# Kernel optimization log

Hardware: AMD Instinct MI355X
Metric: run time of the kernel (lower is better)

The kernel has to match this reference:

```python
import jax, jax.numpy as jnp
import numpy as np


def setup_inputs() -> dict:
    key = jax.random.key(0)
    x = jax.random.normal(key, (4096, 4096), dtype=jnp.float32)
    return {"x": x}


def reference(x):
    """IDXST: y_k = Im{ sum_{n=0}^{N-1} x_n * exp(j*pi*n*(2k+1)/(2N)) }.

    O(N log N) via a 2N-point FFT:
      sum_n x_n e^{j pi n (2k+1)/(2N)} = sum_n (x_n e^{j pi n/(2N)}) e^{j 2 pi n k/(2N)}
    which is the first N entries of an unnormalized 2N-point inverse DFT of the
    twiddled, zero-padded sequence.
    """
    N = x.shape[-1]
    n = jnp.arange(N)
    twiddle = jnp.exp(1j * jnp.pi * n.astype(jnp.float32) / (2.0 * N)).astype(jnp.complex64)
    c = x.astype(jnp.complex64) * twiddle                      # [..., N]
    pad = [(0, 0)] * (x.ndim - 1) + [(0, N)]
    c = jnp.pad(c, pad)                                        # [..., 2N]
    y = jnp.fft.ifft(c, axis=-1) * (2.0 * N)                   # unnormalized IDFT
    return jnp.imag(y[..., :N]).astype(x.dtype)
```

## Files before the change

kernel.cpp:

```cpp
#include <hip/hip_runtime.h>
#include <stdint.h>


#define NN 4096

typedef __attribute__((ext_vector_type(8))) short short8;
typedef __attribute__((ext_vector_type(4))) float f32x4;

__device__ __forceinline__ unsigned short f2bf(float f) {
  unsigned int u = __float_as_uint(f);
  u += 0x7fffu + ((u >> 16) & 1u);
  return (unsigned short)(u >> 16);
}

__device__ __forceinline__ void async_load16(const void* g, void* lds) {
  __builtin_amdgcn_global_load_lds(
      (const __attribute__((address_space(1))) unsigned int*)g,
      (__attribute__((address_space(3))) unsigned int*)lds, 16, 0, 0);
}

#define NXS (NN * NN / 8)
#define NBO (2048 * 2048 / 4)
#define NBP (1024 * 1024 / 4)

__global__ void prep_kernel(const float* __restrict__ x,
                            unsigned short* __restrict__ xo,
                            unsigned short* __restrict__ xee,
                            unsigned short* __restrict__ xeo,
                            unsigned short* __restrict__ Bo,
                            unsigned short* __restrict__ Bp,
                            unsigned short* __restrict__ Bq) {
  int gi = blockIdx.x * blockDim.x + threadIdx.x;
  if (gi < NXS) {
    int g = gi & 511;
    int r = gi >> 9;
    const float4* src = (const float4*)(x + (size_t)r * NN + g * 8);
    float4 v0 = src[0], v1 = src[1];
    ushort4 ov;
    ov.x = f2bf(v0.y); ov.y = f2bf(v0.w); ov.z = f2bf(v1.y); ov.w = f2bf(v1.w);
    *(ushort4*)&xo[(size_t)r * 2048 + g * 4] = ov;
    unsigned int ee = ((unsigned)f2bf(v1.x) << 16) | f2bf(v0.x);
    *(unsigned int*)&xee[(size_t)r * 1024 + g * 2] = ee;
    unsigned int eo = ((unsigned)f2bf(v1.z) << 16) | f2bf(v0.z);
    *(unsigned int*)&xeo[(size_t)r * 1024 + g * 2] = eo;
  } else if (gi < NXS + NBO) {
    int i = gi - NXS;
    int m0 = (i & 511) * 4;
    int c = i >> 9;
    unsigned int tw = 2u * (unsigned)c + 1u;
    const float sc = 3.14159265358979323846f / 8192.0f;
    ushort4 o; unsigned int ph;
    ph = ((unsigned)(2 * (m0 + 0) + 1) * tw) & 16383u; o.x = f2bf(__sinf((float)ph * sc));
    ph = ((unsigned)(2 * (m0 + 1) + 1) * tw) & 16383u; o.y = f2bf(__sinf((float)ph * sc));
    ph = ((unsigned)(2 * (m0 + 2) + 1) * tw) & 16383u; o.z = f2bf(__sinf((float)ph * sc));
    ph = ((unsigned)(2 * (m0 + 3) + 1) * tw) & 16383u; o.w = f2bf(__sinf((float)ph * sc));
    *(ushort4*)&Bo[(size_t)c * 2048 + m0] = o;
  } else if (gi < NXS + NBO + NBP) {
    int i = gi - NXS - NBO;
    int t0 = (i & 255) * 4;
    int c = i >> 8;
    unsigned int tw = 2u * (unsigned)c + 1u;
    const float sc = 3.14159265358979323846f / 2048.0f;
    ushort4 o; unsigned int ph;
    ph = ((unsigned)(t0 + 0) * tw) & 4095u; o.x = f2bf(__sinf((float)ph * sc));
    ph = ((unsigned)(t0 + 1) * tw) & 4095u; o.y = f2bf(__sinf((float)ph * sc));
    ph = ((unsigned)(t0 + 2) * tw) & 4095u; o.z = f2bf(__sinf((float)ph * sc));
    ph = ((unsigned)(t0 + 3) * tw) & 4095u; o.w = f2bf(__sinf((float)ph * sc));
    *(ushort4*)&Bp[(size_t)c * 1024 + t0] = o;
  } else {
    int i = gi - NXS - NBO - NBP;
    int t0 = (i & 255) * 4;
    int c = i >> 8;
    unsigned int tw = 2u * (unsigned)c + 1u;
    const float sc = 3.14159265358979323846f / 4096.0f;
    ushort4 o; unsigned int ph;
    ph = ((unsigned)(2 * (t0 + 0) + 1) * tw) & 8191u; o.x = f2bf(__sinf((float)ph * sc));
    ph = ((unsigned)(2 * (t0 + 1) + 1) * tw) & 8191u; o.y = f2bf(__sinf((float)ph * sc));
    ph = ((unsigned)(2 * (t0 + 2) + 1) * tw) & 8191u; o.z = f2bf(__sinf((float)ph * sc));
    ph = ((unsigned)(2 * (t0 + 3) + 1) * tw) & 8191u; o.w = f2bf(__sinf((float)ph * sc));
    *(ushort4*)&Bq[(size_t)c * 1024 + t0] = o;
  }
}

#define PH_BAR  __builtin_amdgcn_s_barrier()
#define W_LGKM0 asm volatile("s_waitcnt lgkmcnt(0)" ::: "memory")
#define W_VM5   asm volatile("s_waitcnt vmcnt(5)" ::: "memory")
#define W_VM0   asm volatile("s_waitcnt vmcnt(0)" ::: "memory")
#define PRIO1   __builtin_amdgcn_s_setprio(1)
#define PRIO0   __builtin_amdgcn_s_setprio(0)

#define STAGEA_G(Abase, Kc, prow0, koff, off) do {                              \
    const unsigned short* _s =                                                  \
        (Abase) + (size_t)((prow0) + st_r) * (Kc) + (koff) + st_c;              \
    async_load16(_s, &lds[(off) + tid * 8]);                                    \
    async_load16(_s + (size_t)64 * (Kc), &lds[(off) + 4096 + tid * 8]);         \
  } while (0)

#define STAGEB_P(srcp, koff, off)                                               \
    async_load16((srcp) + (koff), &lds[(off) + tid * 8])

#define LOADA_G(base, b, mh) do {                                               \
    const int _ab = (base) + (b) * 16384 + wm * 4096 + (mh) * 2048 + lr * 64;   \
    _Pragma("unroll") for (int _i = 0; _i < 2; ++_i) {                          \
      av[(mh) * 2 + _i][0] = *(const short8*)&lds[_ab + _i * 1024 + cA0];       \
      av[(mh) * 2 + _i][1] = *(const short8*)&lds[_ab + _i * 1024 + cA1];       \
    }                                                                           \
  } while (0)

#define LOADB_U(SET, nh) do {                                                   \
    const int _bb = 65536 + wn * 4096 + (nh) * 2048 + lr * 64;                  \
    _Pragma("unroll") for (int _j = 0; _j < 2; ++_j) {                          \
      SET[_j][0] = *(const short8*)&lds[_bb + _j * 1024 + cA0];                 \
      SET[_j][1] = *(const short8*)&lds[_bb + _j * 1024 + cA1];                 \
    }                                                                           \
  } while (0)

#define LOADB_PQ(SET, base) do {                                                \
    const int _bb = (base) + wn * 2048 + lr * 64;                               \
    _Pragma("unroll") for (int _j = 0; _j < 2; ++_j) {                          \
      SET[_j][0] = *(const short8*)&lds[_bb + _j * 1024 + cA0];                 \
      SET[_j][1] = *(const short8*)&lds[_bb + _j * 1024 + cA1];                 \
    }                                                                           \
  } while (0)

#define MMAQ_U(BS, mh, nh) do {                                                 \
    _Pragma("unroll") for (int _k = 0; _k < 2; ++_k)                            \
    _Pragma("unroll") for (int _i = 0; _i < 2; ++_i)                            \
    _Pragma("unroll") for (int _j = 0; _j < 2; ++_j)                            \
      uacc[(mh) * 2 + _i][(nh) * 2 + _j] =                                      \
          __builtin_amdgcn_mfma_f32_16x16x32_bf16(                              \
              av[(mh) * 2 + _i][_k], BS[_j][_k],                                \
              uacc[(mh) * 2 + _i][(nh) * 2 + _j], 0, 0, 0);                     \
  } while (0)

#define MMAQ_PQ(ACC, BS, mh) do {                                               \
    _Pragma("unroll") for (int _k = 0; _k < 2; ++_k)                            \
    _Pragma("unroll") for (int _i = 0; _i < 2; ++_i)                            \
    _Pragma("unroll") for (int _j = 0; _j < 2; ++_j)                            \
      ACC[(mh) * 2 + _i][_j] =                                                  \
          __builtin_amdgcn_mfma_f32_16x16x32_bf16(                              \
              av[(mh) * 2 + _i][_k], BS[_j][_k],                                \
              ACC[(mh) * 2 + _i][_j], 0, 0, 0);                                 \
  } while (0)

__global__ __launch_bounds__(512) void gemm3_kernel(
    const unsigned short* __restrict__ xo,
    const unsigned short* __restrict__ xee,
    const unsigned short* __restrict__ xeo,
    const unsigned short* __restrict__ Bo,
    const unsigned short* __restrict__ Bp,
    const unsigned short* __restrict__ Bq,
    float* __restrict__ out) {
  __shared__ __align__(16) unsigned short lds[73728];

  const int bx = blockIdx.x;
  const int row0 = (bx & 15) * 256;
  const int c0 = (bx >> 4) * 32;

  const int tid = threadIdx.x;
  const int lane = tid & 63;
  const int wave = tid >> 6;
  const int wm = wave >> 1;
  const int wn = wave & 1;
  const int lr = lane & 15, kq = lane >> 4;
  const int st_r = tid >> 3;
  const int st_c = ((tid & 7) ^ (st_r & 7)) * 8;
  const int cA0 = (kq ^ (lr & 7)) * 8;
  const int cA1 = ((4 + kq) ^ (lr & 7)) * 8;

  const int ru0 = (st_r < 32) ? (c0 + st_r) : (2047 - c0 - (st_r - 32));
  const int ru1 = (st_r < 32) ? (1023 - c0 - st_r) : (1024 + c0 + (st_r - 32));
  const int rpq = (st_r < 32) ? (c0 + st_r) : (1023 - c0 - (st_r - 32));
  const unsigned short* sBo0 = Bo + (size_t)ru0 * 2048 + st_c;
  const unsigned short* sBo1 = Bo + (size_t)ru1 * 2048 + st_c;
  const unsigned short* sBp  = Bp + (size_t)rpq * 1024 + st_c;
  const unsigned short* sBq  = Bq + (size_t)rpq * 1024 + st_c;

  f32x4 uacc[4][4], pacc[4][2], qacc[4][2];
#pragma unroll
  for (int i = 0; i < 4; ++i) {
#pragma unroll
    for (int j = 0; j < 4; ++j) uacc[i][j] = (f32x4){0.f, 0.f, 0.f, 0.f};
#pragma unroll
    for (int j = 0; j < 2; ++j) {
      pacc[i][j] = (f32x4){0.f, 0.f, 0.f, 0.f};
      qacc[i][j] = (f32x4){0.f, 0.f, 0.f, 0.f};
    }
  }
  short8 av[4][2], bv0[2][2], bv1[2][2];

  STAGEA_G(xo, 2048, row0,       0, 0);
  STAGEA_G(xo, 2048, row0 + 128, 0, 8192);
  STAGEB_P(sBo0, 0, 65536);
  STAGEB_P(sBo1, 0, 69632);
  W_VM0; PH_BAR;

  for (int it = 0; it < 15; ++it) {
    const int t64 = it << 7;
    LOADA_G(0, 0, 0); LOADB_U(bv0, 0);
    STAGEA_G(xo, 2048, row0, t64 + 64, 16384);
    PH_BAR; W_LGKM0; PRIO1; MMAQ_U(bv0, 0, 0); PRIO0; PH_BAR;
    LOADB_U(bv1, 1);
    STAGEA_G(xo, 2048, row0 + 128, t64 + 64, 24576);
    PH_BAR; W_LGKM0; PRIO1; MMAQ_U(bv1, 0, 1); PRIO0; PH_BAR;
    LOADA_G(0, 0, 1);
    STAGEB_P(sBo0, t64 + 64, 65536);
    STAGEB_P(sBo1, t64 + 64, 69632);
    PH_BAR; W_LGKM0; PRIO1; MMAQ_U(bv1, 1, 1); PRIO0; PH_BAR;
    PRIO1; MMAQ_U(bv0, 1, 0); PRIO0; W_VM0; PH_BAR;
    LOADA_G(0, 1, 0); LOADB_U(bv0, 0);
    STAGEA_G(xo, 2048, row0, t64 + 128, 0);
    PH_BAR; W_LGKM0; PRIO1; MMAQ_U(bv0, 0, 0); PRIO0; PH_BAR;
    LOADB_U(bv1, 1);
    STAGEA_G(xo, 2048, row0 + 128, t64 + 128, 8192);
    PH_BAR; W_LGKM0; PRIO1; MMAQ_U(bv1, 0, 1); PRIO0; PH_BAR;
    LOADA_G(0, 1, 1);
    STAGEB_P(sBo0, t64 + 128, 65536);
    STAGEB_P(sBo1, t64 + 128, 69632);
    PH_BAR; W_LGKM0; PRIO1; MMAQ_U(bv1, 1, 1); PRIO0; PH_BAR;
    PRIO1; MMAQ_U(bv0, 1, 0); PRIO0; W_VM0; PH_BAR;
  }
  {
    LOADA_G(0, 0, 0); LOADB_U(bv0, 0);
    STAGEA_G(xo, 2048, row0, 1984, 16384);
    PH_BAR; W_LGKM0; PRIO1; MMAQ_U(bv0, 0, 0); PRIO0; PH_BAR;
    LOADB_U(bv1, 1);
    STAGEA_G(xo, 2048, row0 + 128, 1984, 24576);
    PH_BAR; W_LGKM0; PRIO1; MMAQ_U(bv1, 0, 1); PRIO0; PH_BAR;
    LOADA_G(0, 0, 1);
    STAGEB_P(sBo0, 1984, 65536);
    STAGEB_P(sBo1, 1984, 69632);
    PH_BAR; W_LGKM0; PRIO1; MMAQ_U(bv1, 1, 1); PRIO0; PH_BAR;
    PRIO1; MMAQ_U(bv0, 1, 0); PRIO0; W_VM0; PH_BAR;
    LOADA_G(0, 1, 0); LOADB_U(bv0, 0);
    W_LGKM0; PRIO1; MMAQ_U(bv0, 0, 0); PRIO0;
    LOADB_U(bv1, 1);
    W_LGKM0; PRIO1; MMAQ_U(bv1, 0, 1); PRIO0;
    LOADA_G(0, 1, 1);
    W_LGKM0; PRIO1; MMAQ_U(bv1, 1, 1); MMAQ_U(bv0, 1, 0); PRIO0;
  }

  PH_BAR;
  STAGEA_G(xee, 1024, row0,       0, 0);
  STAGEA_G(xee, 1024, row0 + 128, 0, 8192);
  STAGEB_P(sBp, 0, 65536);
  STAGEA_G(xeo, 1024, row0,       0, 32768);
  STAGEA_G(xeo, 1024, row0 + 128, 0, 40960);
  STAGEB_P(sBq, 0, 69632);
  W_VM5; PH_BAR;

#define PQ_TILE(b, kn) do {                                                     \
    LOADA_G(0, b, 0); LOADB_PQ(bv0, 65536);                                     \
    STAGEA_G(xee, 1024, row0, kn, ((b) ^ 1) * 16384);                           \
    PH_BAR; W_LGKM0; PRIO1; MMAQ_PQ(pacc, bv0, 0); PRIO0; PH_BAR;               \
    LOADA_G(0, b, 1);                                                           \
    STAGEA_G(xee, 1024, row0 + 128, kn, ((b) ^ 1) * 16384 + 8192);              \
    STAGEB_P(sBp, kn, 65536);                                                   \
    PH_BAR; W_LGKM0; PRIO1; MMAQ_PQ(pacc, bv0, 1); PRIO0; W_VM5; PH_BAR;        \
    LOADA_G(32768, b, 0); LOADB_PQ(bv1, 69632);                                 \
    STAGEA_G(xeo, 1024, row0, kn, 32768 + ((b) ^ 1) * 16384);                   \
    PH_BAR; W_LGKM0; PRIO1; MMAQ_PQ(qacc, bv1, 0); PRIO0; PH_BAR;               \
    LOADA_G(32768, b, 1);                                                       \
    STAGEA_G(xeo, 1024, row0 + 128, kn, 32768 + ((b) ^ 1) * 16384 + 8192);      \
    STAGEB_P(sBq, kn, 69632);                                                   \
    PH_BAR; W_LGKM0; PRIO1; MMAQ_PQ(qacc, bv1, 1); PRIO0; W_VM5; PH_BAR;        \
  } while (0)

  for (int it = 0; it < 7; ++it) {
    const int t64 = it << 7;
    PQ_TILE(0, t64 + 64);
    PQ_TILE(1, t64 + 128);
  }
  PQ_TILE(0, 960);
  {
    LOADA_G(0, 1, 0); LOADB_PQ(bv0, 65536);
    W_LGKM0; PRIO1; MMAQ_PQ(pacc, bv0, 0); PRIO0;
    LOADA_G(0, 1, 1);
    W_LGKM0; PRIO1; MMAQ_PQ(pacc, bv0, 1); PRIO0; W_VM0; PH_BAR;
    LOADA_G(32768, 1, 0); LOADB_PQ(bv1, 69632);
    W_LGKM0; PRIO1; MMAQ_PQ(qacc, bv1, 0); PRIO0;
    LOADA_G(32768, 1, 1);
    W_LGKM0; PRIO1; MMAQ_PQ(qacc, bv1, 1); PRIO0;
  }
#undef PQ_TILE

#pragma unroll
  for (int i = 0; i < 4; ++i)
#pragma unroll
    for (int j = 0; j < 2; ++j)
#pragma unroll
      for (int rr = 0; rr < 4; ++rr) {
        const int r_out = row0 + wm * 64 + i * 16 + kq * 4 + rr;
        float* orow = out + (size_t)r_out * NN;
        const int cs = j * 16 + lr;
        const float u1 = uacc[i][j][rr];
        const float u4 = uacc[i][j + 2][rr];
        const float pa = pacc[i][j][rr];
        const float qa = qacc[i][j][rr];
        const float v1 = pa + qa;
        const float v2 = qa - pa;
        if (wn == 0) {
          orow[c0 + cs]        = v1 + u1;
          orow[4095 - c0 - cs] = u1 - v1;
          orow[2047 - c0 - cs] = v2 + u4;
          orow[2048 + c0 + cs] = u4 - v2;
        } else {
          orow[1023 - c0 - cs] = v1 + u1;
          orow[3072 + c0 + cs] = u1 - v1;
          orow[1024 + c0 + cs] = v2 + u4;
          orow[3071 - c0 - cs] = u4 - v2;
        }
      }
}

extern "C" void kernel_launch(void* const* d_in, const int* in_sizes, int n_in,
                              void* d_out, int out_size, void* d_ws, size_t ws_size,
                              hipStream_t stream) {
  const float* x = (const float*)d_in[0];
  float* out = (float*)d_out;
  unsigned short* xo  = (unsigned short*)d_ws;
  unsigned short* xee = xo + (size_t)NN * 2048;
  unsigned short* xeo = xee + (size_t)NN * 1024;
  unsigned short* Bo  = xeo + (size_t)NN * 1024;
  unsigned short* Bp  = Bo + (size_t)2048 * 2048;
  unsigned short* Bq  = Bp + (size_t)1024 * 1024;

  int prep_threads = NXS + NBO + 2 * NBP;
  prep_kernel<<<prep_threads / 256, 256, 0, stream>>>(x, xo, xee, xeo, Bo, Bp, Bq);

  gemm3_kernel<<<256, 512, 0, stream>>>(xo, xee, xeo, Bo, Bp, Bq, out);
}
```

Before: 79.58 us.

## Halve GEMM row tile to 128 with 256-thread blocks and sequential P/Q phases

Changes the fused GEMM from 256-row tiles with 8 waves to 128-row tiles with 4 waves, launching 512 blocks instead of 256. LDS usage drops from about 144KB to 48KB, which allows several blocks per CU and fills more CUs. The P and Q phases now run one after another instead of interleaved, with full vmcnt(0) waits in place of the partial vmcnt(5) waits. The trade-off is that each B tile is reused across fewer rows, so more B traffic goes to global memory and L2, and there is less overlap inside each block.

```diff
diff --git a/kernel.cpp b/kernel.cpp
--- a/kernel.cpp
+++ b/kernel.cpp
@@ -84,23 +84,22 @@
 
 #define PH_BAR  __builtin_amdgcn_s_barrier()
 #define W_LGKM0 asm volatile("s_waitcnt lgkmcnt(0)" ::: "memory")
-#define W_VM5   asm volatile("s_waitcnt vmcnt(5)" ::: "memory")
 #define W_VM0   asm volatile("s_waitcnt vmcnt(0)" ::: "memory")
 #define PRIO1   __builtin_amdgcn_s_setprio(1)
 #define PRIO0   __builtin_amdgcn_s_setprio(0)
 
-#define STAGEA_G(Abase, Kc, prow0, koff, off) do {                              \
+#define STAGEA_H(Abase, Kc, prow0, koff, off) do {                              \
     const unsigned short* _s =                                                  \
         (Abase) + (size_t)((prow0) + st_r) * (Kc) + (koff) + st_c;              \
     async_load16(_s, &lds[(off) + tid * 8]);                                    \
-    async_load16(_s + (size_t)64 * (Kc), &lds[(off) + 4096 + tid * 8]);         \
+    async_load16(_s + (size_t)32 * (Kc), &lds[(off) + 2048 + tid * 8]);         \
   } while (0)
 
 #define STAGEB_P(srcp, koff, off)                                               \
     async_load16((srcp) + (koff), &lds[(off) + tid * 8])
 
-#define LOADA_G(base, b, mh) do {                                               \
-    const int _ab = (base) + (b) * 16384 + wm * 4096 + (mh) * 2048 + lr * 64;   \
+#define LOADA(b, mh) do {                                                       \
+    const int _ab = (b) * 8192 + wm * 4096 + (mh) * 2048 + lr * 64;             \
     _Pragma("unroll") for (int _i = 0; _i < 2; ++_i) {                          \
       av[(mh) * 2 + _i][0] = *(const short8*)&lds[_ab + _i * 1024 + cA0];       \
       av[(mh) * 2 + _i][1] = *(const short8*)&lds[_ab + _i * 1024 + cA1];       \
@@ -108,15 +107,15 @@
   } while (0)
 
 #define LOADB_U(SET, nh) do {                                                   \
-    const int _bb = 65536 + wn * 4096 + (nh) * 2048 + lr * 64;                  \
+    const int _bb = 16384 + wn * 4096 + (nh) * 2048 + lr * 64;                  \
     _Pragma("unroll") for (int _j = 0; _j < 2; ++_j) {                          \
       SET[_j][0] = *(const short8*)&lds[_bb + _j * 1024 + cA0];                 \
       SET[_j][1] = *(const short8*)&lds[_bb + _j * 1024 + cA1];                 \
     }                                                                           \
   } while (0)
 
-#define LOADB_PQ(SET, base) do {                                                \
-    const int _bb = (base) + wn * 2048 + lr * 64;                               \
+#define LOADB_PQ(SET) do {                                                      \
+    const int _bb = 16384 + wn * 2048 + lr * 64;                                \
     _Pragma("unroll") for (int _j = 0; _j < 2; ++_j) {                          \
       SET[_j][0] = *(const short8*)&lds[_bb + _j * 1024 + cA0];                 \
       SET[_j][1] = *(const short8*)&lds[_bb + _j * 1024 + cA1];                 \
@@ -143,7 +142,7 @@
               ACC[(mh) * 2 + _i][_j], 0, 0, 0);                                 \
   } while (0)
 
-__global__ __launch_bounds__(512) void gemm3_kernel(
+__global__ __launch_bounds__(256) void gemm3_kernel(
     const unsigned short* __restrict__ xo,
     const unsigned short* __restrict__ xee,
     const unsigned short* __restrict__ xeo,
@@ -151,11 +150,11 @@
     const unsigned short* __restrict__ Bp,
     const unsigned short* __restrict__ Bq,
     float* __restrict__ out) {
-  __shared__ __align__(16) unsigned short lds[73728];
+  __shared__ __align__(16) unsigned short lds[24576];
 
   const int bx = blockIdx.x;
-  const int row0 = (bx & 15) * 256;
-  const int c0 = (bx >> 4) * 32;
+  const int row0 = (bx & 31) * 128;
+  const int c0 = (bx >> 5) * 32;
 
   const int tid = threadIdx.x;
   const int lane = tid & 63;
@@ -168,13 +167,14 @@
   const int cA0 = (kq ^ (lr & 7)) * 8;
   const int cA1 = ((4 + kq) ^ (lr & 7)) * 8;
 
-  const int ru0 = (st_r < 32) ? (c0 + st_r) : (2047 - c0 - (st_r - 32));
-  const int ru1 = (st_r < 32) ? (1023 - c0 - st_r) : (1024 + c0 + (st_r - 32));
-  const int rpq = (st_r < 32) ? (c0 + st_r) : (1023 - c0 - (st_r - 32));
-  const unsigned short* sBo0 = Bo + (size_t)ru0 * 2048 + st_c;
-  const unsigned short* sBo1 = Bo + (size_t)ru1 * 2048 + st_c;
-  const unsigned short* sBp  = Bp + (size_t)rpq * 1024 + st_c;
-  const unsigned short* sBq  = Bq + (size_t)rpq * 1024 + st_c;
+  const unsigned short* sU1 = Bo + (size_t)(c0 + st_r) * 2048 + st_c;
+  const unsigned short* sU4 = Bo + (size_t)(2047 - c0 - st_r) * 2048 + st_c;
+  const unsigned short* sU2 = Bo + (size_t)(1023 - c0 - st_r) * 2048 + st_c;
+  const unsigned short* sU3 = Bo + (size_t)(1024 + c0 + st_r) * 2048 + st_c;
+  const unsigned short* sP1 = Bp + (size_t)(c0 + st_r) * 1024 + st_c;
+  const unsigned short* sP2 = Bp + (size_t)(1023 - c0 - st_r) * 1024 + st_c;
+  const unsigned short* sQ1 = Bq + (size_t)(c0 + st_r) * 1024 + st_c;
+  const unsigned short* sQ2 = Bq + (size_t)(1023 - c0 - st_r) * 1024 + st_c;
 
   f32x4 uacc[4][4], pacc[4][2], qacc[4][2];
 #pragma unroll
@@ -189,100 +189,99 @@
   }
   short8 av[4][2], bv0[2][2], bv1[2][2];
 
-  STAGEA_G(xo, 2048, row0,       0, 0);
-  STAGEA_G(xo, 2048, row0 + 128, 0, 8192);
-  STAGEB_P(sBo0, 0, 65536);
-  STAGEB_P(sBo1, 0, 69632);
+  STAGEA_H(xo, 2048, row0,      0, 0);
+  STAGEA_H(xo, 2048, row0 + 64, 0, 4096);
+  STAGEB_P(sU1, 0, 16384);
+  STAGEB_P(sU4, 0, 18432);
+  STAGEB_P(sU2, 0, 20480);
+  STAGEB_P(sU3, 0, 22528);
   W_VM0; PH_BAR;
 
   for (int it = 0; it < 15; ++it) {
     const int t64 = it << 7;
-    LOADA_G(0, 0, 0); LOADB_U(bv0, 0);
-    STAGEA_G(xo, 2048, row0, t64 + 64, 16384);
+    LOADA(0, 0); LOADB_U(bv0, 0);
+    STAGEA_H(xo, 2048, row0, t64 + 64, 8192);
     PH_BAR; W_LGKM0; PRIO1; MMAQ_U(bv0, 0, 0); PRIO0; PH_BAR;
     LOADB_U(bv1, 1);
-    STAGEA_G(xo, 2048, row0 + 128, t64 + 64, 24576);
+    STAGEA_H(xo, 2048, row0 + 64, t64 + 64, 12288);
     PH_BAR; W_LGKM0; PRIO1; MMAQ_U(bv1, 0, 1); PRIO0; PH_BAR;
-    LOADA_G(0, 0, 1);
-    STAGEB_P(sBo0, t64 + 64, 65536);
-    STAGEB_P(sBo1, t64 + 64, 69632);
+    LOADA(0, 1);
+    STAGEB_P(sU1, t64 + 64, 16384);
+    STAGEB_P(sU4, t64 + 64, 18432);
+    STAGEB_P(sU2, t64 + 64, 20480);
+    STAGEB_P(sU3, t64 + 64, 22528);
     PH_BAR; W_LGKM0; PRIO1; MMAQ_U(bv1, 1, 1); PRIO0; PH_BAR;
     PRIO1; MMAQ_U(bv0, 1, 0); PRIO0; W_VM0; PH_BAR;
-    LOADA_G(0, 1, 0); LOADB_U(bv0, 0);
-    STAGEA_G(xo, 2048, row0, t64 + 128, 0);
+    LOADA(1, 0); LOADB_U(bv0, 0);
+    STAGEA_H(xo, 2048, row0, t64 + 128, 0);
     PH_BAR; W_LGKM0; PRIO1; MMAQ_U(bv0, 0, 0); PRIO0; PH_BAR;
     LOADB_U(bv1, 1);
-    STAGEA_G(xo, 2048, row0 + 128, t64 + 128, 8192);
+    STAGEA_H(xo, 2048, row0 + 64, t64 + 128, 4096);
     PH_BAR; W_LGKM0; PRIO1; MMAQ_U(bv1, 0, 1); PRIO0; PH_BAR;
-    LOADA_G(0, 1, 1);
-    STAGEB_P(sBo0, t64 + 128, 65536);
-    STAGEB_P(sBo1, t64 + 128, 69632);
+    LOADA(1, 1);
+    STAGEB_P(sU1, t64 + 128, 16384);
+    STAGEB_P(sU4, t64 + 128, 18432);
+    STAGEB_P(sU2, t64 + 128, 20480);
+    STAGEB_P(sU3, t64 + 128, 22528);
     PH_BAR; W_LGKM0; PRIO1; MMAQ_U(bv1, 1, 1); PRIO0; PH_BAR;
     PRIO1; MMAQ_U(bv0, 1, 0); PRIO0; W_VM0; PH_BAR;
   }
   {
-    LOADA_G(0, 0, 0); LOADB_U(bv0, 0);
-    STAGEA_G(xo, 2048, row0, 1984, 16384);
+    LOADA(0, 0); LOADB_U(bv0, 0);
+    STAGEA_H(xo, 2048, row0, 1984, 8192);
     PH_BAR; W_LGKM0; PRIO1; MMAQ_U(bv0, 0, 0); PRIO0; PH_BAR;
     LOADB_U(bv1, 1);
-    STAGEA_G(xo, 2048, row0 + 128, 1984, 24576);
+    STAGEA_H(xo, 2048, row0 + 64, 1984, 12288);
     PH_BAR; W_LGKM0; PRIO1; MMAQ_U(bv1, 0, 1); PRIO0; PH_BAR;
-    LOADA_G(0, 0, 1);
-    STAGEB_P(sBo0, 1984, 65536);
-    STAGEB_P(sBo1, 1984, 69632);
+    LOADA(0, 1);
+    STAGEB_P(sU1, 1984, 16384);
+    STAGEB_P(sU4, 1984, 18432);
+    STAGEB_P(sU2, 1984, 20480);
+    STAGEB_P(sU3, 1984, 22528);
     PH_BAR; W_LGKM0; PRIO1; MMAQ_U(bv1, 1, 1); PRIO0; PH_BAR;
     PRIO1; MMAQ_U(bv0, 1, 0); PRIO0; W_VM0; PH_BAR;
-    LOADA_G(0, 1, 0); LOADB_U(bv0, 0);
+    LOADA(1, 0); LOADB_U(bv0, 0);
     W_LGKM0; PRIO1; MMAQ_U(bv0, 0, 0); PRIO0;
     LOADB_U(bv1, 1);
     W_LGKM0; PRIO1; MMAQ_U(bv1, 0, 1); PRIO0;
-    LOADA_G(0, 1, 1);
+    LOADA(1, 1);
     W_LGKM0; PRIO1; MMAQ_U(bv1, 1, 1); MMAQ_U(bv0, 1, 0); PRIO0;
   }
 
-  PH_BAR;
-  STAGEA_G(xee, 1024, row0,       0, 0);
-  STAGEA_G(xee, 1024, row0 + 128, 0, 8192);
-  STAGEB_P(sBp, 0, 65536);
-  STAGEA_G(xeo, 1024, row0,       0, 32768);
-  STAGEA_G(xeo, 1024, row0 + 128, 0, 40960);
-  STAGEB_P(sBq, 0, 69632);
-  W_VM5; PH_BAR;
-
-#define PQ_TILE(b, kn) do {                                                     \
-    LOADA_G(0, b, 0); LOADB_PQ(bv0, 65536);                                     \
-    STAGEA_G(xee, 1024, row0, kn, ((b) ^ 1) * 16384);                           \
-    PH_BAR; W_LGKM0; PRIO1; MMAQ_PQ(pacc, bv0, 0); PRIO0; PH_BAR;               \
-    LOADA_G(0, b, 1);                                                           \
-    STAGEA_G(xee, 1024, row0 + 128, kn, ((b) ^ 1) * 16384 + 8192);              \
-    STAGEB_P(sBp, kn, 65536);                                                   \
-    PH_BAR; W_LGKM0; PRIO1; MMAQ_PQ(pacc, bv0, 1); PRIO0; W_VM5; PH_BAR;        \
-    LOADA_G(32768, b, 0); LOADB_PQ(bv1, 69632);                                 \
-    STAGEA_G(xeo, 1024, row0, kn, 32768 + ((b) ^ 1) * 16384);                   \
-    PH_BAR; W_LGKM0; PRIO1; MMAQ_PQ(qacc, bv1, 0); PRIO0; PH_BAR;               \
-    LOADA_G(32768, b, 1);                                                       \
-    STAGEA_G(xeo, 1024, row0 + 128, kn, 32768 + ((b) ^ 1) * 16384 + 8192);      \
-    STAGEB_P(sBq, kn, 69632);                                                   \
-    PH_BAR; W_LGKM0; PRIO1; MMAQ_PQ(qacc, bv1, 1); PRIO0; W_VM5; PH_BAR;        \
-  } while (0)
-
-  for (int it = 0; it < 7; ++it) {
-    const int t64 = it << 7;
-    PQ_TILE(0, t64 + 64);
-    PQ_TILE(1, t64 + 128);
-  }
-  PQ_TILE(0, 960);
-  {
-    LOADA_G(0, 1, 0); LOADB_PQ(bv0, 65536);
-    W_LGKM0; PRIO1; MMAQ_PQ(pacc, bv0, 0); PRIO0;
-    LOADA_G(0, 1, 1);
-    W_LGKM0; PRIO1; MMAQ_PQ(pacc, bv0, 1); PRIO0; W_VM0; PH_BAR;
-    LOADA_G(32768, 1, 0); LOADB_PQ(bv1, 69632);
-    W_LGKM0; PRIO1; MMAQ_PQ(qacc, bv1, 0); PRIO0;
-    LOADA_G(32768, 1, 1);
-    W_LGKM0; PRIO1; MMAQ_PQ(qacc, bv1, 1); PRIO0;
-  }
+#define PQ_TILE(ACC, Asrc, s1, s2, b, kn) do {                                  \
+    LOADA(b, 0); LOADB_PQ(bv0);                                                 \
+    STAGEA_H(Asrc, 1024, row0, kn, ((b) ^ 1) * 8192);                           \
+    PH_BAR; W_LGKM0; PRIO1; MMAQ_PQ(ACC, bv0, 0); PRIO0; PH_BAR;                \
+    LOADA(b, 1);                                                                \
+    STAGEA_H(Asrc, 1024, row0 + 64, kn, ((b) ^ 1) * 8192 + 4096);               \
+    STAGEB_P(s1, kn, 16384);                                                    \
+    STAGEB_P(s2, kn, 18432);                                                    \
+    PH_BAR; W_LGKM0; PRIO1; MMAQ_PQ(ACC, bv0, 1); PRIO0; W_VM0; PH_BAR;         \
+  } while (0)
+
+#define PQ_SEG(ACC, Asrc, s1, s2) do {                                          \
+    PH_BAR;                                                                     \
+    STAGEA_H(Asrc, 1024, row0,      0, 0);                                      \
+    STAGEA_H(Asrc, 1024, row0 + 64, 0, 4096);                                   \
+    STAGEB_P(s1, 0, 16384);                                                     \
+    STAGEB_P(s2, 0, 18432);                                                     \
+    W_VM0; PH_BAR;                                                              \
+    for (int it = 0; it < 7; ++it) {                                            \
+      const int t64 = it << 7;                                                  \
+      PQ_TILE(ACC, Asrc, s1, s2, 0, t64 + 64);                                  \
+      PQ_TILE(ACC, Asrc, s1, s2, 1, t64 + 128);                                 \
+    }                                                                           \
+    PQ_TILE(ACC, Asrc, s1, s2, 0, 960);                                         \
+    LOADA(1, 0); LOADB_PQ(bv0);                                                 \
+    W_LGKM0; PRIO1; MMAQ_PQ(ACC, bv0, 0); PRIO0;                                \
+    LOADA(1, 1);                                                                \
+    W_LGKM0; PRIO1; MMAQ_PQ(ACC, bv0, 1); PRIO0;                                \
+  } while (0)
+
+  PQ_SEG(pacc, xee, sP1, sP2);
+  PQ_SEG(qacc, xeo, sQ1, sQ2);
 #undef PQ_TILE
+#undef PQ_SEG
 
 #pragma unroll
   for (int i = 0; i < 4; ++i)
@@ -328,5 +327,5 @@
   int prep_threads = NXS + NBO + 2 * NBP;
   prep_kernel<<<prep_threads / 256, 256, 0, stream>>>(x, xo, xee, xeo, Bo, Bp, Bq);
 
-  gemm3_kernel<<<256, 512, 0, stream>>>(xo, xee, xeo, Bo, Bp, Bq, out);
-}
+  gemm3_kernel<<<512, 256, 0, stream>>>(xo, xee, xeo, Bo, Bp, Bq, out);
+}
```

Measured after the change: 119.4 us. 1.5x slower.

## Load A operand directly from global into registers, stage only B in LDS

Applied to the files above, without the earlier changes.

The A (signal) operand is no longer staged through LDS. Each wave now loads its rows straight from global memory into registers, prefetching the next k-slice while the MFMAs for the current one run. Only the B (trig basis) tiles are double-buffered in LDS, which shrinks shared memory from 144KB to 32KB. The P and Q GEMM phases now run one after the other instead of interleaved. The intent is fewer LDS round trips and barriers, plus room for higher occupancy. The cost is that global loads are uncoalesced (16B per lane with a row stride) and their latency is hidden only by one slice of MFMAs.

```diff
diff --git a/kernel.cpp b/kernel.cpp
--- a/kernel.cpp
+++ b/kernel.cpp
@@ -83,64 +83,51 @@
 }
 
 #define PH_BAR  __builtin_amdgcn_s_barrier()
-#define W_LGKM0 asm volatile("s_waitcnt lgkmcnt(0)" ::: "memory")
-#define W_VM5   asm volatile("s_waitcnt vmcnt(5)" ::: "memory")
+#define W_VM2   asm volatile("s_waitcnt vmcnt(2)" ::: "memory")
 #define W_VM0   asm volatile("s_waitcnt vmcnt(0)" ::: "memory")
 #define PRIO1   __builtin_amdgcn_s_setprio(1)
 #define PRIO0   __builtin_amdgcn_s_setprio(0)
 
-#define STAGEA_G(Abase, Kc, prow0, koff, off) do {                              \
-    const unsigned short* _s =                                                  \
-        (Abase) + (size_t)((prow0) + st_r) * (Kc) + (koff) + st_c;              \
-    async_load16(_s, &lds[(off) + tid * 8]);                                    \
-    async_load16(_s + (size_t)64 * (Kc), &lds[(off) + 4096 + tid * 8]);         \
-  } while (0)
-
 #define STAGEB_P(srcp, koff, off)                                               \
     async_load16((srcp) + (koff), &lds[(off) + tid * 8])
 
-#define LOADA_G(base, b, mh) do {                                               \
-    const int _ab = (base) + (b) * 16384 + wm * 4096 + (mh) * 2048 + lr * 64;   \
-    _Pragma("unroll") for (int _i = 0; _i < 2; ++_i) {                          \
-      av[(mh) * 2 + _i][0] = *(const short8*)&lds[_ab + _i * 1024 + cA0];       \
-      av[(mh) * 2 + _i][1] = *(const short8*)&lds[_ab + _i * 1024 + cA1];       \
+#define U_TILE(b, kn) do {                                                      \
+    { const int _bb = (b) * 8192 + wn * 4096 + lr * 64;                         \
+      _Pragma("unroll") for (int _j = 0; _j < 4; ++_j) {                        \
+        bv[_j][0] = *(const short8*)&lds[_bb + _j * 1024 + cA0];                \
+        bv[_j][1] = *(const short8*)&lds[_bb + _j * 1024 + cA1];                \
+      } }                                                                       \
+    STAGEB_P(sU0, kn, ((b) ^ 1) * 8192);                                        \
+    STAGEB_P(sU1, kn, ((b) ^ 1) * 8192 + 4096);                                 \
+    PRIO1;                                                                      \
+    _Pragma("unroll") for (int _i = 0; _i < 4; ++_i) {                          \
+      _Pragma("unroll") for (int _k = 0; _k < 2; ++_k)                          \
+      _Pragma("unroll") for (int _j = 0; _j < 4; ++_j)                          \
+        uacc[_i][_j] = __builtin_amdgcn_mfma_f32_16x16x32_bf16(                 \
+            av[_i][_k], bv[_j][_k], uacc[_i][_j], 0, 0, 0);                     \
+      av[_i][0] = *(const short8*)(aU + (size_t)_i * 32768 + (kn));             \
+      av[_i][1] = *(const short8*)(aU + (size_t)_i * 32768 + (kn) + 32);        \
     }                                                                           \
+    PRIO0; W_VM2; PH_BAR;                                                       \
   } while (0)
 
-#define LOADB_U(SET, nh) do {                                                   \
-    const int _bb = 65536 + wn * 4096 + (nh) * 2048 + lr * 64;                  \
-    _Pragma("unroll") for (int _j = 0; _j < 2; ++_j) {                          \
-      SET[_j][0] = *(const short8*)&lds[_bb + _j * 1024 + cA0];                 \
-      SET[_j][1] = *(const short8*)&lds[_bb + _j * 1024 + cA1];                 \
+#define PQ_TILE(ACC, aPtr, sPtr, b, kn) do {                                    \
+    { const int _bb = (b) * 8192 + wn * 2048 + lr * 64;                         \
+      _Pragma("unroll") for (int _j = 0; _j < 2; ++_j) {                        \
+        bvp[_j][0] = *(const short8*)&lds[_bb + _j * 1024 + cA0];               \
+        bvp[_j][1] = *(const short8*)&lds[_bb + _j * 1024 + cA1];               \
+      } }                                                                       \
+    STAGEB_P(sPtr, kn, ((b) ^ 1) * 8192);                                       \
+    PRIO1;                                                                      \
+    _Pragma("unroll") for (int _i = 0; _i < 4; ++_i) {                          \
+      _Pragma("unroll") for (int _k = 0; _k < 2; ++_k)                          \
+      _Pragma("unroll") for (int _j = 0; _j < 2; ++_j)                          \
+        ACC[_i][_j] = __builtin_amdgcn_mfma_f32_16x16x32_bf16(                  \
+            av[_i][_k], bvp[_j][_k], ACC[_i][_j], 0, 0, 0);                     \
+      av[_i][0] = *(const short8*)((aPtr) + (size_t)_i * 16384 + (kn));         \
+      av[_i][1] = *(const short8*)((aPtr) + (size_t)_i * 16384 + (kn) + 32);    \
     }                                                                           \
-  } while (0)
-
-#define LOADB_PQ(SET, base) do {                                                \
-    const int _bb = (base) + wn * 2048 + lr * 64;                               \
-    _Pragma("unroll") for (int _j = 0; _j < 2; ++_j) {                          \
-      SET[_j][0] = *(const short8*)&lds[_bb + _j * 1024 + cA0];                 \
-      SET[_j][1] = *(const short8*)&lds[_bb + _j * 1024 + cA1];                 \
-    }                                                                           \
-  } while (0)
-
-#define MMAQ_U(BS, mh, nh) do {                                                 \
-    _Pragma("unroll") for (int _k = 0; _k < 2; ++_k)                            \
-    _Pragma("unroll") for (int _i = 0; _i < 2; ++_i)                            \
-    _Pragma("unroll") for (int _j = 0; _j < 2; ++_j)                            \
-      uacc[(mh) * 2 + _i][(nh) * 2 + _j] =                                      \
-          __builtin_amdgcn_mfma_f32_16x16x32_bf16(                              \
-              av[(mh) * 2 + _i][_k], BS[_j][_k],                                \
-              uacc[(mh) * 2 + _i][(nh) * 2 + _j], 0, 0, 0);                     \
-  } while (0)
-
-#define MMAQ_PQ(ACC, BS, mh) do {                                               \
-    _Pragma("unroll") for (int _k = 0; _k < 2; ++_k)                            \
-    _Pragma("unroll") for (int _i = 0; _i < 2; ++_i)                            \
-    _Pragma("unroll") for (int _j = 0; _j < 2; ++_j)                            \
-      ACC[(mh) * 2 + _i][_j] =                                                  \
-          __builtin_amdgcn_mfma_f32_16x16x32_bf16(                              \
-              av[(mh) * 2 + _i][_k], BS[_j][_k],                                \
-              ACC[(mh) * 2 + _i][_j], 0, 0, 0);                                 \
+    PRIO0; W_VM2; PH_BAR;                                                       \
   } while (0)
 
 __global__ __launch_bounds__(512) void gemm3_kernel(
@@ -151,7 +138,7 @@
     const unsigned short* __restrict__ Bp,
     const unsigned short* __restrict__ Bq,
     float* __restrict__ out) {
-  __shared__ __align__(16) unsigned short lds[73728];
+  __shared__ __align__(16) unsigned short lds[16384];
 
   const int bx = blockIdx.x;
   const int row0 = (bx & 15) * 256;
@@ -168,13 +155,18 @@
   const int cA0 = (kq ^ (lr & 7)) * 8;
   const int cA1 = ((4 + kq) ^ (lr & 7)) * 8;
 
+  const int arow = row0 + wm * 64 + lr;
+  const unsigned short* aU = xo  + (size_t)arow * 2048 + kq * 8;
+  const unsigned short* aP = xee + (size_t)arow * 1024 + kq * 8;
+  const unsigned short* aQ = xeo + (size_t)arow * 1024 + kq * 8;
+
   const int ru0 = (st_r < 32) ? (c0 + st_r) : (2047 - c0 - (st_r - 32));
   const int ru1 = (st_r < 32) ? (1023 - c0 - st_r) : (1024 + c0 + (st_r - 32));
   const int rpq = (st_r < 32) ? (c0 + st_r) : (1023 - c0 - (st_r - 32));
-  const unsigned short* sBo0 = Bo + (size_t)ru0 * 2048 + st_c;
-  const unsigned short* sBo1 = Bo + (size_t)ru1 * 2048 + st_c;
-  const unsigned short* sBp  = Bp + (size_t)rpq * 1024 + st_c;
-  const unsigned short* sBq  = Bq + (size_t)rpq * 1024 + st_c;
+  const unsigned short* sU0 = Bo + (size_t)ru0 * 2048 + st_c;
+  const unsigned short* sU1 = Bo + (size_t)ru1 * 2048 + st_c;
+  const unsigned short* sP  = Bp + (size_t)rpq * 1024 + st_c;
+  const unsigned short* sQ  = Bq + (size_t)rpq * 1024 + st_c;
 
   f32x4 uacc[4][4], pacc[4][2], qacc[4][2];
 #pragma unroll
@@ -187,102 +179,105 @@
       qacc[i][j] = (f32x4){0.f, 0.f, 0.f, 0.f};
     }
   }
-  short8 av[4][2], bv0[2][2], bv1[2][2];
-
-  STAGEA_G(xo, 2048, row0,       0, 0);
-  STAGEA_G(xo, 2048, row0 + 128, 0, 8192);
-  STAGEB_P(sBo0, 0, 65536);
-  STAGEB_P(sBo1, 0, 69632);
+  short8 av[4][2], bv[4][2], bvp[2][2];
+
+  STAGEB_P(sU0, 0, 0);
+  STAGEB_P(sU1, 0, 4096);
+#pragma unroll
+  for (int i = 0; i < 4; ++i) {
+    av[i][0] = *(const short8*)(aU + (size_t)i * 32768);
+    av[i][1] = *(const short8*)(aU + (size_t)i * 32768 + 32);
+  }
   W_VM0; PH_BAR;
 
   for (int it = 0; it < 15; ++it) {
     const int t64 = it << 7;
-    LOADA_G(0, 0, 0); LOADB_U(bv0, 0);
-    STAGEA_G(xo, 2048, row0, t64 + 64, 16384);
-    PH_BAR; W_LGKM0; PRIO1; MMAQ_U(bv0, 0, 0); PRIO0; PH_BAR;
-    LOADB_U(bv1, 1);
-    STAGEA_G(xo, 2048, row0 + 128, t64 + 64, 24576);
-    PH_BAR; W_LGKM0; PRIO1; MMAQ_U(bv1, 0, 1); PRIO0; PH_BAR;
-    LOADA_G(0, 0, 1);
-    STAGEB_P(sBo0, t64 + 64, 65536);
-    STAGEB_P(sBo1, t64 + 64, 69632);
-    PH_BAR; W_LGKM0; PRIO1; MMAQ_U(bv1, 1, 1); PRIO0; PH_BAR;
-    PRIO1; MMAQ_U(bv0, 1, 0); PRIO0; W_VM0; PH_BAR;
-    LOADA_G(0, 1, 0); LOADB_U(bv0, 0);
-    STAGEA_G(xo, 2048, row0, t64 + 128, 0);
-    PH_BAR; W_LGKM0; PRIO1; MMAQ_U(bv0, 0, 0); PRIO0; PH_BAR;
-    LOADB_U(bv1, 1);
-    STAGEA_G(xo, 2048, row0 + 128, t64 + 128, 8192);
-    PH_BAR; W_LGKM0; PRIO1; MMAQ_U(bv1, 0, 1); PRIO0; PH_BAR;
-    LOADA_G(0, 1, 1);
-    STAGEB_P(sBo0, t64 + 128, 65536);
-    STAGEB_P(sBo1, t64 + 128, 69632);
-    PH_BAR; W_LGKM0; PRIO1; MMAQ_U(bv1, 1, 1); PRIO0; PH_BAR;
-    PRIO1; MMAQ_U(bv0, 1, 0); PRIO0; W_VM0; PH_BAR;
-  }
+    U_TILE(0, t64 + 64);
+    U_TILE(1, t64 + 128);
+  }
+  U_TILE(0, 1984);
   {
-    LOADA_G(0, 0, 0); LOADB_U(bv0, 0);
-    STAGEA_G(xo, 2048, row0, 1984, 16384);
-    PH_BAR; W_LGKM0; PRIO1; MMAQ_U(bv0, 0, 0); PRIO0; PH_BAR;
-    LOADB_U(bv1, 1);
-    STAGEA_G(xo, 2048, row0 + 128, 1984, 24576);
-    PH_BAR; W_LGKM0; PRIO1; MMAQ_U(bv1, 0, 1); PRIO0; PH_BAR;
-    LOADA_G(0, 0, 1);
-    STAGEB_P(sBo0, 1984, 65536);
-    STAGEB_P(sBo1, 1984, 69632);
-    PH_BAR; W_LGKM0; PRIO1; MMAQ_U(bv1, 1, 1); PRIO0; PH_BAR;
-    PRIO1; MMAQ_U(bv0, 1, 0); PRIO0; W_VM0; PH_BAR;
-    LOADA_G(0, 1, 0); LOADB_U(bv0, 0);
-    W_LGKM0; PRIO1; MMAQ_U(bv0, 0, 0); PRIO0;
-    LOADB_U(bv1, 1);
-    W_LGKM0; PRIO1; MMAQ_U(bv1, 0, 1); PRIO0;
-    LOADA_G(0, 1, 1);
-    W_LGKM0; PRIO1; MMAQ_U(bv1, 1, 1); MMAQ_U(bv0, 1, 0); PRIO0;
-  }
-
-  PH_BAR;
-  STAGEA_G(xee, 1024, row0,       0, 0);
-  STAGEA_G(xee, 1024, row0 + 128, 0, 8192);
-  STAGEB_P(sBp, 0, 65536);
-  STAGEA_G(xeo, 1024, row0,       0, 32768);
-  STAGEA_G(xeo, 1024, row0 + 128, 0, 40960);
-  STAGEB_P(sBq, 0, 69632);
-  W_VM5; PH_BAR;
-
-#define PQ_TILE(b, kn) do {                                                     \
-    LOADA_G(0, b, 0); LOADB_PQ(bv0, 65536);                                     \
-    STAGEA_G(xee, 1024, row0, kn, ((b) ^ 1) * 16384);                           \
-    PH_BAR; W_LGKM0; PRIO1; MMAQ_PQ(pacc, bv0, 0); PRIO0; PH_BAR;               \
-    LOADA_G(0, b, 1);                                                           \
-    STAGEA_G(xee, 1024, row0 + 128, kn, ((b) ^ 1) * 16384 + 8192);              \
-    STAGEB_P(sBp, kn, 65536);                                                   \
-    PH_BAR; W_LGKM0; PRIO1; MMAQ_PQ(pacc, bv0, 1); PRIO0; W_VM5; PH_BAR;        \
-    LOADA_G(32768, b, 0); LOADB_PQ(bv1, 69632);                                 \
-    STAGEA_G(xeo, 1024, row0, kn, 32768 + ((b) ^ 1) * 16384);                   \
-    PH_BAR; W_LGKM0; PRIO1; MMAQ_PQ(qacc, bv1, 0); PRIO0; PH_BAR;               \
-    LOADA_G(32768, b, 1);                                                       \
-    STAGEA_G(xeo, 1024, row0 + 128, kn, 32768 + ((b) ^ 1) * 16384 + 8192);      \
-    STAGEB_P(sBq, kn, 69632);                                                   \
-    PH_BAR; W_LGKM0; PRIO1; MMAQ_PQ(qacc, bv1, 1); PRIO0; W_VM5; PH_BAR;        \
-  } while (0)
-
+    const int _bb = 8192 + wn * 4096 + lr * 64;
+#pragma unroll
+    for (int _j = 0; _j < 4; ++_j) {
+      bv[_j][0] = *(const short8*)&lds[_bb + _j * 1024 + cA0];
+      bv[_j][1] = *(const short8*)&lds[_bb + _j * 1024 + cA1];
+    }
+    PRIO1;
+#pragma unroll
+    for (int _i = 0; _i < 4; ++_i)
+#pragma unroll
+      for (int _k = 0; _k < 2; ++_k)
+#pragma unroll
+        for (int _j = 0; _j < 4; ++_j)
+          uacc[_i][_j] = __builtin_amdgcn_mfma_f32_16x16x32_bf16(
+              av[_i][_k], bv[_j][_k], uacc[_i][_j], 0, 0, 0);
+    PRIO0;
+  }
+
+  STAGEB_P(sP, 0, 0);
+#pragma unroll
+  for (int i = 0; i < 4; ++i) {
+    av[i][0] = *(const short8*)(aP + (size_t)i * 16384);
+    av[i][1] = *(const short8*)(aP + (size_t)i * 16384 + 32);
+  }
+  W_VM0; PH_BAR;
   for (int it = 0; it < 7; ++it) {
     const int t64 = it << 7;
-    PQ_TILE(0, t64 + 64);
-    PQ_TILE(1, t64 + 128);
-  }
-  PQ_TILE(0, 960);
+    PQ_TILE(pacc, aP, sP, 0, t64 + 64);
+    PQ_TILE(pacc, aP, sP, 1, t64 + 128);
+  }
+  PQ_TILE(pacc, aP, sP, 0, 960);
   {
-    LOADA_G(0, 1, 0); LOADB_PQ(bv0, 65536);
-    W_LGKM0; PRIO1; MMAQ_PQ(pacc, bv0, 0); PRIO0;
-    LOADA_G(0, 1, 1);
-    W_LGKM0; PRIO1; MMAQ_PQ(pacc, bv0, 1); PRIO0; W_VM0; PH_BAR;
-    LOADA_G(32768, 1, 0); LOADB_PQ(bv1, 69632);
-    W_LGKM0; PRIO1; MMAQ_PQ(qacc, bv1, 0); PRIO0;
-    LOADA_G(32768, 1, 1);
-    W_LGKM0; PRIO1; MMAQ_PQ(qacc, bv1, 1); PRIO0;
-  }
-#undef PQ_TILE
+    const int _bb = 8192 + wn * 2048 + lr * 64;
+#pragma unroll
+    for (int _j = 0; _j < 2; ++_j) {
+      bvp[_j][0] = *(const short8*)&lds[_bb + _j * 1024 + cA0];
+      bvp[_j][1] = *(const short8*)&lds[_bb + _j * 1024 + cA1];
+    }
+    PRIO1;
+#pragma unroll
+    for (int _i = 0; _i < 4; ++_i)
+#pragma unroll
+      for (int _k = 0; _k < 2; ++_k)
+#pragma unroll
+        for (int _j = 0; _j < 2; ++_j)
+          pacc[_i][_j] = __builtin_amdgcn_mfma_f32_16x16x32_bf16(
+              av[_i][_k], bvp[_j][_k], pacc[_i][_j], 0, 0, 0);
+    PRIO0;
+  }
+
+  STAGEB_P(sQ, 0, 0);
+#pragma unroll
+  for (int i = 0; i < 4; ++i) {
+    av[i][0] = *(const short8*)(aQ + (size_t)i * 16384);
+    av[i][1] = *(const short8*)(aQ + (size_t)i * 16384 + 32);
+  }
+  W_VM0; PH_BAR;
+  for (int it = 0; it < 7; ++it) {
+    const int t64 = it << 7;
+    PQ_TILE(qacc, aQ, sQ, 0, t64 + 64);
+    PQ_TILE(qacc, aQ, sQ, 1, t64 + 128);
+  }
+  PQ_TILE(qacc, aQ, sQ, 0, 960);
+  {
+    const int _bb = 8192 + wn * 2048 + lr * 64;
+#pragma unroll
+    for (int _j = 0; _j < 2; ++_j) {
+      bvp[_j][0] = *(const short8*)&lds[_bb + _j * 1024 + cA0];
+      bvp[_j][1] = *(const short8*)&lds[_bb + _j * 1024 + cA1];
+    }
+    PRIO1;
+#pragma unroll
+    for (int _i = 0; _i < 4; ++_i)
+#pragma unroll
+      for (int _k = 0; _k < 2; ++_k)
+#pragma unroll
+        for (int _j = 0; _j < 2; ++_j)
+          qacc[_i][_j] = __builtin_amdgcn_mfma_f32_16x16x32_bf16(
+              av[_i][_k], bvp[_j][_k], qacc[_i][_j], 0, 0, 0);
+    PRIO0;
+  }
 
 #pragma unroll
   for (int i = 0; i < 4; ++i)
```

Result: slower. 174.6 us (+119.4%).
